# Kernel optimization log

Hardware: AMD Instinct MI355X
Metric: run time of the kernel (lower is better)

## Reference

```python
import jax, jax.numpy as jnp
import numpy as np

B, C, CI, HM, HC = 4, 64, 32, 128, 64  # batch, in_channels, inter_channels, main HW, cross HW
BN_EPS = 1e-5


def conv1x1(x, w, b):
    # x: [B,Cin,H,W], w: [Cout,Cin], b: [Cout]
    return jnp.einsum('bchw,oc->bohw', x, w) + b[None, :, None, None]


def _lin_coords(n_in, n_out):
    # PyTorch bilinear, align_corners=False: src = (i+0.5)*scale - 0.5, clamped
    scale = n_in / n_out
    src = (jnp.arange(n_out, dtype=jnp.float32) + 0.5) * scale - 0.5
    src = jnp.clip(src, 0.0, n_in - 1)
    i0 = jnp.floor(src).astype(jnp.int32)
    i1 = jnp.minimum(i0 + 1, n_in - 1)
    w = src - i0.astype(jnp.float32)
    return i0, i1, w


def resize_bilinear(x, h_out, w_out):
    # x: [B,C,H,W] -> [B,C,h_out,w_out], matches torch F.interpolate(mode='bilinear', align_corners=False)
    _, _, h_in, w_in = x.shape
    i0, i1, wh = _lin_coords(h_in, h_out)
    x = x[:, :, i0, :] * (1.0 - wh)[None, None, :, None] + x[:, :, i1, :] * wh[None, None, :, None]
    j0, j1, ww = _lin_coords(w_in, w_out)
    x = x[:, :, :, j0] * (1.0 - ww)[None, None, None, :] + x[:, :, :, j1] * ww[None, None, None, :]
    return x


def setup_inputs() -> dict:
    key = jax.random.key(0)
    ks = jax.random.split(key, 12)
    p = lambda k, shape, s=0.05: jax.random.normal(k, shape, dtype=jnp.float32) * s
    return {
        'main_feature': jax.random.normal(ks[0], (B, C, HM, HM), dtype=jnp.float32),
        'cross_feature': jax.random.normal(ks[1], (B, C, HC, HC), dtype=jnp.float32),
        'g_w': p(ks[2], (CI, C)), 'g_b': p(ks[3], (CI,)),
        'theta_w': p(ks[4], (CI, C)), 'theta_b': p(ks[5], (CI,)),
        'phi_w': p(ks[6], (CI, C)), 'phi_b': p(ks[7], (CI,)),
        'w_w': p(ks[8], (C, CI)), 'w_b': p(ks[9], (C,)),
        'bn_gamma': 1.0 + p(ks[10], (C,)), 'bn_beta': p(ks[11], (C,)),
    }


def reference(main_feature, cross_feature, g_w, g_b, theta_w, theta_b,
              phi_w, phi_b, w_w, w_b, bn_gamma, bn_beta):
    b, _, hc, wc = cross_feature.shape
    hm = main_feature.shape[2]
    # g(cross) -> [B, Nc, Ci]
    x = conv1x1(cross_feature, g_w, g_b).reshape(b, CI, -1).transpose(0, 2, 1)
    # theta(cross) -> [B, Ci, Nc]
    y = conv1x1(cross_feature, theta_w, theta_b).reshape(b, CI, -1)
    # phi(resize(main -> cross size)) -> [B, Nc, Ci]
    z = resize_bilinear(main_feature, hc, hc)
    z = conv1x1(z, phi_w, phi_b).reshape(b, CI, -1).transpose(0, 2, 1)
    # unscaled attention: [B, Nc, Nc]
    f = jnp.einsum('bnc,bcm->bnm', x, y)
    attn = jax.nn.softmax(f, axis=-1)
    out = jnp.einsum('bnm,bmc->bnc', attn, z)           # [B, Nc, Ci]
    out = out.transpose(0, 2, 1).reshape(b, CI, hc, wc)  # [B, Ci, Hc, Wc]
    # W: 1x1 conv + BatchNorm2d (training mode: batch statistics, biased var)
    out = conv1x1(out, w_w, w_b)
    mean = out.mean(axis=(0, 2, 3), keepdims=True)
    var = out.var(axis=(0, 2, 3), keepdims=True)
    out = (out - mean) * jax.lax.rsqrt(var + BN_EPS)
    out = out * bn_gamma[None, :, None, None] + bn_beta[None, :, None, None]
    out = resize_bilinear(out, hm, hm)
    return out + main_feature
```

## Files before the change

### kernel.cpp

```cpp
#include <hip/hip_runtime.h>
#include <hip/hip_bf16.h>


typedef __attribute__((ext_vector_type(8))) short bf16x8;
typedef __attribute__((ext_vector_type(4))) float f32x4;

#define LOG2E 1.4426950408889634f

static __device__ __forceinline__ unsigned short f2bf_bits(float x) {
    __hip_bfloat16 h = __float2bfloat16(x);
    return *(unsigned short*)&h;
}
static __device__ __forceinline__ unsigned int pk2bf(float a, float b) {
    __hip_bfloat162 h = __float22bfloat162_rn(make_float2(a, b));
    return *(unsigned int*)&h;
}

__global__ __launch_bounds__(256) void qkv_kernel(
    const float* __restrict__ cross, const float* __restrict__ mainf,
    const float* __restrict__ g_w,  const float* __restrict__ g_b,
    const float* __restrict__ th_w, const float* __restrict__ th_b,
    const float* __restrict__ ph_w, const float* __restrict__ ph_b,
    __hip_bfloat16* __restrict__ Qb, __hip_bfloat16* __restrict__ Kb,
    __hip_bfloat16* __restrict__ Vt)
{
    __shared__ float xs[64][128];
    const int kind = blockIdx.x >> 7;
    const int sub  = blockIdx.x & 127;
    const int b    = sub >> 5;
    const int n0   = (sub & 31) << 7;
    const int tid  = threadIdx.x;
    const float* w  = (kind == 0) ? g_w : (kind == 1) ? th_w : ph_w;
    const float* bs = (kind == 0) ? g_b : (kind == 1) ? th_b : ph_b;

    if (kind < 2) {
        const float* src = cross + (((size_t)(b * 64)) << 12) + n0;
        const int jr = (tid & 31) << 2, c0 = tid >> 5;
#pragma unroll
        for (int it = 0; it < 8; ++it) {
            int c = (it << 3) | c0;
            *(float4*)&xs[c][jr] = *(const float4*)(src + ((size_t)c << 12) + jr);
        }
    } else {
        const int px = tid & 127, chh = tid >> 7;
        const int n = n0 + px;
        const int i2 = (n >> 6) << 1, j2 = (n & 63) << 1;
        const float* src = mainf + (((size_t)(b * 64)) << 14) + i2 * 128 + j2;
#pragma unroll 4
        for (int cc = 0; cc < 32; ++cc) {
            int c = (chh << 5) | cc;
            const float2 a = *(const float2*)(src + ((size_t)c << 14));
            const float2 d = *(const float2*)(src + ((size_t)c << 14) + 128);
            xs[c][px] = 0.25f * ((a.x + a.y) + (d.x + d.y));
        }
    }
    __syncthreads();

    const int px = tid & 127, cih = tid >> 7, ci0 = cih << 4;
    float acc[16];
#pragma unroll
    for (int j = 0; j < 16; ++j) acc[j] = bs[ci0 + j];
#pragma unroll 4
    for (int c = 0; c < 64; ++c) {
        float x = xs[c][px];
#pragma unroll
        for (int j = 0; j < 16; ++j)
            acc[j] = fmaf(w[((ci0 + j) << 6) + c], x, acc[j]);
    }
    const int n = n0 + px;
    const int pix = (b << 12) + n;
    if (kind < 2) {
        if (kind == 0) {
#pragma unroll
            for (int j = 0; j < 16; ++j) acc[j] *= LOG2E;
        }
        unsigned int u[8];
#pragma unroll
        for (int i = 0; i < 8; ++i)
            u[i] = (unsigned int)f2bf_bits(acc[2 * i]) |
                   ((unsigned int)f2bf_bits(acc[2 * i + 1]) << 16);
        uint4* d4 = (uint4*)(((kind == 0) ? Qb : Kb) + (size_t)pix * 32 + ci0);
        d4[0] = make_uint4(u[0], u[1], u[2], u[3]);
        d4[1] = make_uint4(u[4], u[5], u[6], u[7]);
    } else {
#pragma unroll
        for (int j = 0; j < 16; ++j)
            Vt[((size_t)((b << 5) | (ci0 + j)) << 12) + n] = __float2bfloat16(acc[j]);
    }
}

__global__ __launch_bounds__(256) void attn_mfma(
    const __hip_bfloat16* __restrict__ Qb, const __hip_bfloat16* __restrict__ Kb,
    const __hip_bfloat16* __restrict__ Vt, const float* __restrict__ w_w,
    const float* __restrict__ w_b, float* __restrict__ out2)
{
    __shared__ __align__(16) __hip_bfloat16 pbuf[4][2][16][40];
    __shared__ __align__(16) float redbuf[3][64][12];
    __shared__ __align__(16) float obuf[16][36];
    const int tid = threadIdx.x, lane = tid & 63, w = tid >> 6;
    const int lo = lane & 15, c = lane >> 4;
    const int b = blockIdx.y, qbase = blockIdx.x << 4;

    const bf16x8 aq = *(const bf16x8*)(Qb + (((size_t)(b << 12) + qbase + lo) << 5) + (c << 3));
    const __hip_bfloat16* Kbb = Kb + ((size_t)(b << 12) << 5);
    const __hip_bfloat16* Vbb = Vt + ((size_t)(b << 5) << 12);

    f32x4 acc0 = {0.f,0.f,0.f,0.f}, acc1 = {0.f,0.f,0.f,0.f};
    float den = 0.f;
    const f32x4 z = {0.f,0.f,0.f,0.f};
    const int kq = w << 10;
#define LDK(k)      (*(const bf16x8*)(Kbb + ((size_t)((k) + lo) << 5) + (c << 3)))
#define LDV(k, cio) (*(const bf16x8*)(Vbb + ((size_t)(lo + (cio)) << 12) + (k) + (c << 3)))

    bf16x8 k0c = LDK(kq),      k1c = LDK(kq + 16);
    bf16x8 vB0 = LDV(kq, 0),   vB1 = LDV(kq, 16);
    bf16x8 k0n = LDK(kq + 32), k1n = LDK(kq + 48);
    bf16x8 vN0 = LDV(kq + 32, 0), vN1 = LDV(kq + 32, 16);
    bf16x8 ap;

    {
        f32x4 s0 = __builtin_amdgcn_mfma_f32_16x16x32_bf16(k0c, aq, z, 0, 0, 0);
        f32x4 s1 = __builtin_amdgcn_mfma_f32_16x16x32_bf16(k1c, aq, z, 0, 0, 0);
        float p0 = __builtin_amdgcn_exp2f(s0[0]), p1 = __builtin_amdgcn_exp2f(s0[1]);
        float p2 = __builtin_amdgcn_exp2f(s0[2]), p3 = __builtin_amdgcn_exp2f(s0[3]);
        float q0 = __builtin_amdgcn_exp2f(s1[0]), q1 = __builtin_amdgcn_exp2f(s1[1]);
        float q2 = __builtin_amdgcn_exp2f(s1[2]), q3 = __builtin_amdgcn_exp2f(s1[3]);
        den += ((p0 + p1) + (p2 + p3)) + ((q0 + q1) + (q2 + q3));
        uint2 wv0 = make_uint2(pk2bf(p0, p1), pk2bf(p2, p3));
        uint2 wv1 = make_uint2(pk2bf(q0, q1), pk2bf(q2, q3));
        *(uint2*)&pbuf[w][0][lo][c << 2]        = wv0;
        *(uint2*)&pbuf[w][0][lo][16 + (c << 2)] = wv1;
        ap = *(const bf16x8*)&pbuf[w][0][lo][c << 3];
    }

#pragma unroll 2
    for (int ch = 1; ch < 32; ++ch) {
        const int kn = kq + ((ch + 1) & 31) * 32;
        bf16x8 vA0 = vB0, vA1 = vB1;
        vB0 = vN0; vB1 = vN1;
        k0c = k0n; k1c = k1n;
        k0n = LDK(kn); k1n = LDK(kn + 16);
        vN0 = LDV(kn, 0); vN1 = LDV(kn, 16);

        f32x4 s0 = __builtin_amdgcn_mfma_f32_16x16x32_bf16(k0c, aq, z, 0, 0, 0);
        f32x4 s1 = __builtin_amdgcn_mfma_f32_16x16x32_bf16(k1c, aq, z, 0, 0, 0);
        float p0 = __builtin_amdgcn_exp2f(s0[0]), p1 = __builtin_amdgcn_exp2f(s0[1]);
        float p2 = __builtin_amdgcn_exp2f(s0[2]), p3 = __builtin_amdgcn_exp2f(s0[3]);
        float q0 = __builtin_amdgcn_exp2f(s1[0]), q1 = __builtin_amdgcn_exp2f(s1[1]);
        float q2 = __builtin_amdgcn_exp2f(s1[2]), q3 = __builtin_amdgcn_exp2f(s1[3]);
        den += ((p0 + p1) + (p2 + p3)) + ((q0 + q1) + (q2 + q3));
        uint2 wv0 = make_uint2(pk2bf(p0, p1), pk2bf(p2, p3));
        uint2 wv1 = make_uint2(pk2bf(q0, q1), pk2bf(q2, q3));
        *(uint2*)&pbuf[w][ch & 1][lo][c << 2]        = wv0;
        *(uint2*)&pbuf[w][ch & 1][lo][16 + (c << 2)] = wv1;

        acc0 = __builtin_amdgcn_mfma_f32_16x16x32_bf16(ap, vA0, acc0, 0, 0, 0);
        acc1 = __builtin_amdgcn_mfma_f32_16x16x32_bf16(ap, vA1, acc1, 0, 0, 0);

        ap = *(const bf16x8*)&pbuf[w][ch & 1][lo][c << 3];
    }
    acc0 = __builtin_amdgcn_mfma_f32_16x16x32_bf16(ap, vB0, acc0, 0, 0, 0);
    acc1 = __builtin_amdgcn_mfma_f32_16x16x32_bf16(ap, vB1, acc1, 0, 0, 0);
#undef LDK
#undef LDV

    den += __shfl_xor(den, 16);
    den += __shfl_xor(den, 32);

    if (w) {
        f32x4* rb = (f32x4*)&redbuf[w - 1][lane][0];
        rb[0] = acc0; rb[1] = acc1;
        f32x4 dv = {den, 0.f, 0.f, 0.f};
        rb[2] = dv;
    }
    __syncthreads();
    if (w == 0) {
#pragma unroll
        for (int ww = 0; ww < 3; ++ww) {
            const f32x4* rb = (const f32x4*)&redbuf[ww][lane][0];
            f32x4 a0 = rb[0], a1 = rb[1], dv = rb[2];
            acc0 += a0; acc1 += a1;
            den += dv[0];
        }
#pragma unroll
        for (int r = 0; r < 4; ++r) {
            float inv = 1.0f / __shfl(den, (c << 2) | r);
            obuf[(c << 2) | r][lo]      = acc0[r] * inv;
            obuf[(c << 2) | r][16 + lo] = acc1[r] * inv;
        }
    }
    __syncthreads();

    const int q = tid & 15, cog = tid >> 4;
    float ov[32];
    const float4* orow = (const float4*)&obuf[q][0];
#pragma unroll
    for (int k4 = 0; k4 < 8; ++k4) {
        float4 t = orow[k4];
        ov[4*k4] = t.x; ov[4*k4+1] = t.y; ov[4*k4+2] = t.z; ov[4*k4+3] = t.w;
    }
    float* dstbase = out2 + (((size_t)(b << 6)) << 12) + qbase + q;
#pragma unroll
    for (int kk = 0; kk < 4; ++kk) {
        int co = (kk << 4) | cog;
        const float4* wr = (const float4*)&w_w[co << 5];
        float acc = w_b[co];
#pragma unroll
        for (int k4 = 0; k4 < 8; ++k4) {
            float4 t = wr[k4];
            acc = fmaf(t.x, ov[4*k4],   acc);
            acc = fmaf(t.y, ov[4*k4+1], acc);
            acc = fmaf(t.z, ov[4*k4+2], acc);
            acc = fmaf(t.w, ov[4*k4+3], acc);
        }
        dstbase[(size_t)co << 12] = acc;
    }
}

__global__ __launch_bounds__(256) void stats_kernel(
    const float* __restrict__ out2, float* __restrict__ stats1)
{
    int co = blockIdx.x >> 2, b = blockIdx.x & 3, t = threadIdx.x;
    const float* p = out2 + ((size_t)((b << 6) | co) << 12);
    float s = 0.f, s2 = 0.f;
#pragma unroll
    for (int ii = 0; ii < 16; ++ii) {
        float v = p[(ii << 8) | t];
        s += v; s2 = fmaf(v, v, s2);
    }
    __shared__ float rs[256], rs2[256];
    rs[t] = s; rs2[t] = s2;
    __syncthreads();
    for (int off = 128; off > 0; off >>= 1) {
        if (t < off) { rs[t] += rs[t + off]; rs2[t] += rs2[t + off]; }
        __syncthreads();
    }
    if (t == 0) {
        stats1[blockIdx.x * 2]     = rs[0];
        stats1[blockIdx.x * 2 + 1] = rs2[0];
    }
}

__global__ __launch_bounds__(256) void up_kernel(
    const float* __restrict__ out2, const float* __restrict__ stats1,
    const float* __restrict__ gamma, const float* __restrict__ beta,
    const float* __restrict__ mainf, float* __restrict__ out)
{
    int gid = blockIdx.x * 256 + threadIdx.x;
    int j4 = (gid & 31) << 2;
    int i  = (gid >> 5) & 127;
    int co = (gid >> 12) & 63;
    int b  = gid >> 18;

    float sm = 0.f, sq = 0.f;
#pragma unroll
    for (int bb = 0; bb < 4; ++bb) {
        sm += stats1[((co << 2) | bb) * 2];
        sq += stats1[((co << 2) | bb) * 2 + 1];
    }
    float mean = sm * (1.0f / 16384.0f);
    float var  = sq * (1.0f / 16384.0f) - mean * mean;
    float inv  = rsqrtf(var + 1e-5f);
    float scale = gamma[co] * inv;
    float shift = beta[co] - mean * scale;

    int ih = i >> 1;
    int k0, k1; float wi;
    if (i & 1)       { k0 = ih;     k1 = (ih < 63) ? ih + 1 : 63; wi = 0.25f; }
    else if (ih == 0){ k0 = 0;      k1 = 0;                       wi = 0.0f;  }
    else             { k0 = ih - 1; k1 = ih;                      wi = 0.75f; }

    const float* p0r = out2 + ((size_t)((b << 6) | co) << 12) + (k0 << 6);
    const float* p1r = out2 + ((size_t)((b << 6) | co) << 12) + (k1 << 6);

    float res[4];
#pragma unroll
    for (int jj = 0; jj < 4; ++jj) {
        int j = j4 | jj;
        int il = j >> 1;
        int l0, l1; float wj;
        if (j & 1)       { l0 = il;     l1 = (il < 63) ? il + 1 : 63; wj = 0.25f; }
        else if (il == 0){ l0 = 0;      l1 = 0;                       wj = 0.0f;  }
        else             { l0 = il - 1; l1 = il;                      wj = 0.75f; }
        float v00 = p0r[l0], v01 = p0r[l1];
        float v10 = p1r[l0], v11 = p1r[l1];
        float top = v00 + wj * (v01 - v00);
        float bot = v10 + wj * (v11 - v10);
        float v = top + wi * (bot - top);
        res[jj] = fmaf(v, scale, shift);
    }
    size_t idx = (((size_t)((b << 6) | co)) << 14) + (i << 7) + j4;
    float4 m4 = *(const float4*)(mainf + idx);
    *(float4*)(out + idx) = make_float4(res[0] + m4.x, res[1] + m4.y,
                                        res[2] + m4.z, res[3] + m4.w);
}

extern "C" void kernel_launch(void* const* d_in, const int* in_sizes, int n_in,
                              void* d_out, int out_size, void* d_ws, size_t ws_size,
                              hipStream_t stream)
{
    const float* mainf = (const float*)d_in[0];
    const float* cross = (const float*)d_in[1];
    const float* g_w   = (const float*)d_in[2];
    const float* g_b   = (const float*)d_in[3];
    const float* th_w  = (const float*)d_in[4];
    const float* th_b  = (const float*)d_in[5];
    const float* ph_w  = (const float*)d_in[6];
    const float* ph_b  = (const float*)d_in[7];
    const float* w_w   = (const float*)d_in[8];
    const float* w_b   = (const float*)d_in[9];
    const float* gamma = (const float*)d_in[10];
    const float* beta  = (const float*)d_in[11];
    float* out = (float*)d_out;

    __hip_bfloat16* Qb = (__hip_bfloat16*)d_ws;
    __hip_bfloat16* Kb = Qb + 524288;
    __hip_bfloat16* Vt = Kb + 524288;
    float* out2   = (float*)(Vt + 524288);
    float* stats1 = out2 + 1048576;

    qkv_kernel<<<384, 256, 0, stream>>>(cross, mainf, g_w, g_b, th_w, th_b,
                                        ph_w, ph_b, Qb, Kb, Vt);
    attn_mfma<<<dim3(256, 4), 256, 0, stream>>>(Qb, Kb, Vt, w_w, w_b, out2);
    stats_kernel<<<256, 256, 0, stream>>>(out2, stats1);
    up_kernel<<<4096, 256, 0, stream>>>(out2, stats1, gamma, beta, mainf, out);
}
```

Measured before the change: 168.0 us.

## Switch attention to 32x32x16 MFMA with register-resident P and K-row permutation

Result: faster. 147.3 us (-12.3%).

```diff
diff --git a/kernel.cpp b/kernel.cpp
--- a/kernel.cpp
+++ b/kernel.cpp
@@ -4,6 +4,7 @@
 
 typedef __attribute__((ext_vector_type(8))) short bf16x8;
 typedef __attribute__((ext_vector_type(4))) float f32x4;
+typedef __attribute__((ext_vector_type(16))) float f32x16;
 
 #define LOG2E 1.4426950408889634f
 
@@ -94,126 +95,143 @@
     const __hip_bfloat16* __restrict__ Vt, const float* __restrict__ w_w,
     const float* __restrict__ w_b, float* __restrict__ out2)
 {
-    __shared__ __align__(16) __hip_bfloat16 pbuf[4][2][16][40];
-    __shared__ __align__(16) float redbuf[3][64][12];
-    __shared__ __align__(16) float obuf[16][36];
+    __shared__ __align__(16) float redbuf[3][64][20];
+    __shared__ __align__(16) float obuf[32][36];
     const int tid = threadIdx.x, lane = tid & 63, w = tid >> 6;
-    const int lo = lane & 15, c = lane >> 4;
-    const int b = blockIdx.y, qbase = blockIdx.x << 4;
-
-    const bf16x8 aq = *(const bf16x8*)(Qb + (((size_t)(b << 12) + qbase + lo) << 5) + (c << 3));
+    const int q = lane & 31, h = lane >> 5;
+    const int b = blockIdx.y, qbase = blockIdx.x << 5;
+    const int sig = (q & ~12) | ((q & 4) << 1) | ((q & 8) >> 1);
+
+    const __hip_bfloat16* Qrow = Qb + (((size_t)(b << 12) + qbase + q) << 5);
+    const bf16x8 bq1 = *(const bf16x8*)(Qrow + 8 * h);
+    const bf16x8 bq2 = *(const bf16x8*)(Qrow + 16 + 8 * h);
+
     const __hip_bfloat16* Kbb = Kb + ((size_t)(b << 12) << 5);
-    const __hip_bfloat16* Vbb = Vt + ((size_t)(b << 5) << 12);
-
-    f32x4 acc0 = {0.f,0.f,0.f,0.f}, acc1 = {0.f,0.f,0.f,0.f};
+    const __hip_bfloat16* Vbb = Vt + ((size_t)(b << 5) << 12) + ((size_t)q << 12);
+    const int kq = w << 10;
+#define LDK1(k) (*(const bf16x8*)(Kbb + ((size_t)((k) + sig) << 5) + 8 * h))
+#define LDK2(k) (*(const bf16x8*)(Kbb + ((size_t)((k) + sig) << 5) + 16 + 8 * h))
+#define LDV1(k) (*(const bf16x8*)(Vbb + (k) + 8 * h))
+#define LDV2(k) (*(const bf16x8*)(Vbb + (k) + 16 + 8 * h))
+
+    f32x16 acc;
+#pragma unroll
+    for (int r = 0; r < 16; ++r) acc[r] = 0.f;
+    const f32x16 z16 = acc;
     float den = 0.f;
-    const f32x4 z = {0.f,0.f,0.f,0.f};
-    const int kq = w << 10;
-#define LDK(k)      (*(const bf16x8*)(Kbb + ((size_t)((k) + lo) << 5) + (c << 3)))
-#define LDV(k, cio) (*(const bf16x8*)(Vbb + ((size_t)(lo + (cio)) << 12) + (k) + (c << 3)))
-
-    bf16x8 k0c = LDK(kq),      k1c = LDK(kq + 16);
-    bf16x8 vB0 = LDV(kq, 0),   vB1 = LDV(kq, 16);
-    bf16x8 k0n = LDK(kq + 32), k1n = LDK(kq + 48);
-    bf16x8 vN0 = LDV(kq + 32, 0), vN1 = LDV(kq + 32, 16);
-    bf16x8 ap;
+
+    bf16x8 a1c = LDK1(kq),      a2c = LDK2(kq);
+    bf16x8 v1B = LDV1(kq),      v2B = LDV2(kq);
+    bf16x8 a1n = LDK1(kq + 32), a2n = LDK2(kq + 32);
+    bf16x8 v1N = LDV1(kq + 32), v2N = LDV2(kq + 32);
+    bf16x8 ap1, ap2, v1A, v2A;
 
     {
-        f32x4 s0 = __builtin_amdgcn_mfma_f32_16x16x32_bf16(k0c, aq, z, 0, 0, 0);
-        f32x4 s1 = __builtin_amdgcn_mfma_f32_16x16x32_bf16(k1c, aq, z, 0, 0, 0);
-        float p0 = __builtin_amdgcn_exp2f(s0[0]), p1 = __builtin_amdgcn_exp2f(s0[1]);
-        float p2 = __builtin_amdgcn_exp2f(s0[2]), p3 = __builtin_amdgcn_exp2f(s0[3]);
-        float q0 = __builtin_amdgcn_exp2f(s1[0]), q1 = __builtin_amdgcn_exp2f(s1[1]);
-        float q2 = __builtin_amdgcn_exp2f(s1[2]), q3 = __builtin_amdgcn_exp2f(s1[3]);
-        den += ((p0 + p1) + (p2 + p3)) + ((q0 + q1) + (q2 + q3));
-        uint2 wv0 = make_uint2(pk2bf(p0, p1), pk2bf(p2, p3));
-        uint2 wv1 = make_uint2(pk2bf(q0, q1), pk2bf(q2, q3));
-        *(uint2*)&pbuf[w][0][lo][c << 2]        = wv0;
-        *(uint2*)&pbuf[w][0][lo][16 + (c << 2)] = wv1;
-        ap = *(const bf16x8*)&pbuf[w][0][lo][c << 3];
+        f32x16 s = __builtin_amdgcn_mfma_f32_32x32x16_bf16(a1c, bq1, z16, 0, 0, 0);
+        s = __builtin_amdgcn_mfma_f32_32x32x16_bf16(a2c, bq2, s, 0, 0, 0);
+        float e[16];
+#pragma unroll
+        for (int r = 0; r < 16; ++r) e[r] = __builtin_amdgcn_exp2f(s[r]);
+        den += (((e[0]+e[1])+(e[2]+e[3])) + ((e[4]+e[5])+(e[6]+e[7])))
+             + (((e[8]+e[9])+(e[10]+e[11])) + ((e[12]+e[13])+(e[14]+e[15])));
+        uint4 t1 = make_uint4(pk2bf(e[0],e[1]), pk2bf(e[2],e[3]),
+                              pk2bf(e[4],e[5]), pk2bf(e[6],e[7]));
+        uint4 t2 = make_uint4(pk2bf(e[8],e[9]), pk2bf(e[10],e[11]),
+                              pk2bf(e[12],e[13]), pk2bf(e[14],e[15]));
+        ap1 = *(bf16x8*)&t1; ap2 = *(bf16x8*)&t2;
     }
 
 #pragma unroll 2
     for (int ch = 1; ch < 32; ++ch) {
         const int kn = kq + ((ch + 1) & 31) * 32;
-        bf16x8 vA0 = vB0, vA1 = vB1;
-        vB0 = vN0; vB1 = vN1;
-        k0c = k0n; k1c = k1n;
-        k0n = LDK(kn); k1n = LDK(kn + 16);
-        vN0 = LDV(kn, 0); vN1 = LDV(kn, 16);
-
-        f32x4 s0 = __builtin_amdgcn_mfma_f32_16x16x32_bf16(k0c, aq, z, 0, 0, 0);
-        f32x4 s1 = __builtin_amdgcn_mfma_f32_16x16x32_bf16(k1c, aq, z, 0, 0, 0);
-        float p0 = __builtin_amdgcn_exp2f(s0[0]), p1 = __builtin_amdgcn_exp2f(s0[1]);
-        float p2 = __builtin_amdgcn_exp2f(s0[2]), p3 = __builtin_amdgcn_exp2f(s0[3]);
-        float q0 = __builtin_amdgcn_exp2f(s1[0]), q1 = __builtin_amdgcn_exp2f(s1[1]);
-        float q2 = __builtin_amdgcn_exp2f(s1[2]), q3 = __builtin_amdgcn_exp2f(s1[3]);
-        den += ((p0 + p1) + (p2 + p3)) + ((q0 + q1) + (q2 + q3));
-        uint2 wv0 = make_uint2(pk2bf(p0, p1), pk2bf(p2, p3));
-        uint2 wv1 = make_uint2(pk2bf(q0, q1), pk2bf(q2, q3));
-        *(uint2*)&pbuf[w][ch & 1][lo][c << 2]        = wv0;
-        *(uint2*)&pbuf[w][ch & 1][lo][16 + (c << 2)] = wv1;
-
-        acc0 = __builtin_amdgcn_mfma_f32_16x16x32_bf16(ap, vA0, acc0, 0, 0, 0);
-        acc1 = __builtin_amdgcn_mfma_f32_16x16x32_bf16(ap, vA1, acc1, 0, 0, 0);
-
-        ap = *(const bf16x8*)&pbuf[w][ch & 1][lo][c << 3];
-    }
-    acc0 = __builtin_amdgcn_mfma_f32_16x16x32_bf16(ap, vB0, acc0, 0, 0, 0);
-    acc1 = __builtin_amdgcn_mfma_f32_16x16x32_bf16(ap, vB1, acc1, 0, 0, 0);
-#undef LDK
-#undef LDV
-
-    den += __shfl_xor(den, 16);
+        v1A = v1B; v2A = v2B;
+        v1B = v1N; v2B = v2N;
+        a1c = a1n; a2c = a2n;
+        a1n = LDK1(kn); a2n = LDK2(kn);
+        v1N = LDV1(kn); v2N = LDV2(kn);
+
+        f32x16 s = __builtin_amdgcn_mfma_f32_32x32x16_bf16(a1c, bq1, z16, 0, 0, 0);
+        s = __builtin_amdgcn_mfma_f32_32x32x16_bf16(a2c, bq2, s, 0, 0, 0);
+
+        acc = __builtin_amdgcn_mfma_f32_32x32x16_bf16(ap1, v1A, acc, 0, 0, 0);
+        acc = __builtin_amdgcn_mfma_f32_32x32x16_bf16(ap2, v2A, acc, 0, 0, 0);
+
+        float e[16];
+#pragma unroll
+        for (int r = 0; r < 16; ++r) e[r] = __builtin_amdgcn_exp2f(s[r]);
+        den += (((e[0]+e[1])+(e[2]+e[3])) + ((e[4]+e[5])+(e[6]+e[7])))
+             + (((e[8]+e[9])+(e[10]+e[11])) + ((e[12]+e[13])+(e[14]+e[15])));
+        uint4 t1 = make_uint4(pk2bf(e[0],e[1]), pk2bf(e[2],e[3]),
+                              pk2bf(e[4],e[5]), pk2bf(e[6],e[7]));
+        uint4 t2 = make_uint4(pk2bf(e[8],e[9]), pk2bf(e[10],e[11]),
+                              pk2bf(e[12],e[13]), pk2bf(e[14],e[15]));
+        ap1 = *(bf16x8*)&t1; ap2 = *(bf16x8*)&t2;
+    }
+    acc = __builtin_amdgcn_mfma_f32_32x32x16_bf16(ap1, v1B, acc, 0, 0, 0);
+    acc = __builtin_amdgcn_mfma_f32_32x32x16_bf16(ap2, v2B, acc, 0, 0, 0);
+#undef LDK1
+#undef LDK2
+#undef LDV1
+#undef LDV2
+
     den += __shfl_xor(den, 32);
 
     if (w) {
-        f32x4* rb = (f32x4*)&redbuf[w - 1][lane][0];
-        rb[0] = acc0; rb[1] = acc1;
-        f32x4 dv = {den, 0.f, 0.f, 0.f};
-        rb[2] = dv;
+        float* rb = &redbuf[w - 1][lane][0];
+        f32x4* rb4 = (f32x4*)rb;
+#pragma unroll
+        for (int p = 0; p < 4; ++p) {
+            f32x4 t = {acc[4*p], acc[4*p+1], acc[4*p+2], acc[4*p+3]};
+            rb4[p] = t;
+        }
+        rb[16] = den;
     }
     __syncthreads();
     if (w == 0) {
 #pragma unroll
         for (int ww = 0; ww < 3; ++ww) {
-            const f32x4* rb = (const f32x4*)&redbuf[ww][lane][0];
-            f32x4 a0 = rb[0], a1 = rb[1], dv = rb[2];
-            acc0 += a0; acc1 += a1;
-            den += dv[0];
-        }
-#pragma unroll
-        for (int r = 0; r < 4; ++r) {
-            float inv = 1.0f / __shfl(den, (c << 2) | r);
-            obuf[(c << 2) | r][lo]      = acc0[r] * inv;
-            obuf[(c << 2) | r][16 + lo] = acc1[r] * inv;
+            const float* rb = &redbuf[ww][lane][0];
+            const f32x4* rb4 = (const f32x4*)rb;
+#pragma unroll
+            for (int p = 0; p < 4; ++p) {
+                f32x4 t = rb4[p];
+                acc[4*p] += t[0]; acc[4*p+1] += t[1];
+                acc[4*p+2] += t[2]; acc[4*p+3] += t[3];
+            }
+            den += rb[16];
+        }
+#pragma unroll
+        for (int r = 0; r < 16; ++r) {
+            int qr = (r & 3) + 8 * (r >> 2) + 4 * h;
+            float inv = 1.0f / __shfl(den, qr);
+            obuf[qr][q] = acc[r] * inv;
         }
     }
     __syncthreads();
 
-    const int q = tid & 15, cog = tid >> 4;
+    const int qq = tid & 31, cog = tid >> 5;
     float ov[32];
-    const float4* orow = (const float4*)&obuf[q][0];
+    const float4* orow = (const float4*)&obuf[qq][0];
 #pragma unroll
     for (int k4 = 0; k4 < 8; ++k4) {
         float4 t = orow[k4];
         ov[4*k4] = t.x; ov[4*k4+1] = t.y; ov[4*k4+2] = t.z; ov[4*k4+3] = t.w;
     }
-    float* dstbase = out2 + (((size_t)(b << 6)) << 12) + qbase + q;
-#pragma unroll
-    for (int kk = 0; kk < 4; ++kk) {
-        int co = (kk << 4) | cog;
+    float* dstbase = out2 + (((size_t)(b << 6)) << 12) + qbase + qq;
+#pragma unroll
+    for (int kk = 0; kk < 8; ++kk) {
+        int co = (kk << 3) | cog;
         const float4* wr = (const float4*)&w_w[co << 5];
-        float acc = w_b[co];
+        float acc2 = w_b[co];
 #pragma unroll
         for (int k4 = 0; k4 < 8; ++k4) {
             float4 t = wr[k4];
-            acc = fmaf(t.x, ov[4*k4],   acc);
-            acc = fmaf(t.y, ov[4*k4+1], acc);
-            acc = fmaf(t.z, ov[4*k4+2], acc);
-            acc = fmaf(t.w, ov[4*k4+3], acc);
-        }
-        dstbase[(size_t)co << 12] = acc;
+            acc2 = fmaf(t.x, ov[4*k4],   acc2);
+            acc2 = fmaf(t.y, ov[4*k4+1], acc2);
+            acc2 = fmaf(t.z, ov[4*k4+2], acc2);
+            acc2 = fmaf(t.w, ov[4*k4+3], acc2);
+        }
+        dstbase[(size_t)co << 12] = acc2;
     }
 }
 
@@ -321,7 +339,7 @@
 
     qkv_kernel<<<384, 256, 0, stream>>>(cross, mainf, g_w, g_b, th_w, th_b,
                                         ph_w, ph_b, Qb, Kb, Vt);
-    attn_mfma<<<dim3(256, 4), 256, 0, stream>>>(Qb, Kb, Vt, w_w, w_b, out2);
+    attn_mfma<<<dim3(128, 4), 256, 0, stream>>>(Qb, Kb, Vt, w_w, w_b, out2);
     stats_kernel<<<256, 256, 0, stream>>>(out2, stats1);
     up_kernel<<<4096, 256, 0, stream>>>(out2, stats1, gamma, beta, mainf, out);
 }
```
